# Kernel tuning notes

Measured on AMD Instinct MI355X. Metric: run time of the kernel, lower is better.

## Reference

```python
import jax, jax.numpy as jnp
import numpy as np

B, Lq, Lk, E = 4, 512, 512, 128
D = 2 * E  # input feature dim = 2*encode_size


def setup_inputs() -> dict:
    key = jax.random.key(0)
    ks = jax.random.split(key, 6)
    return {
        "query": jax.random.normal(ks[0], (B, Lq, D), jnp.float32),
        "key": jax.random.normal(ks[1], (B, Lk, D), jnp.float32),
        "value": jax.random.normal(ks[2], (B, Lq, D), jnp.float32),
        "Wc1": jax.random.normal(ks[3], (D, E), jnp.float32) / np.sqrt(D),
        "Wc2": jax.random.normal(ks[4], (D, E), jnp.float32) / np.sqrt(D),
        "vc": jax.random.normal(ks[5], (E,), jnp.float32) / np.sqrt(E),
    }


def reference(query, key, value, Wc1, Wc2, vc):
    # q: [B, Lq, E], k: [B, Lk, E]
    q = query @ Wc1
    k = key @ Wc2
    # additive (Bahdanau) scores: tanh(q + k) reduced by vc -> [B, Lk, Lq]
    sjt = jnp.einsum('blqe,e->blq', jnp.tanh(q[:, None, :, :] + k[:, :, None, :]), vc)
    atten = jax.nn.softmax(sjt, axis=2)  # softmax over Lq (dim=2), dropout p=0.0 is identity
    context = jnp.einsum('blq,bqd->bld', atten, value)  # [B, Lk, D]
    return (context, atten)
```

## Files before the change

### kernel.cpp

```cpp
#include <hip/hip_runtime.h>

#define NB 4
#define LQ 512
#define LK 512
#define EE 128
#define DD 256

__device__ __forceinline__ float fast_rcp(float x) { return __builtin_amdgcn_rcpf(x); }

__global__ __launch_bounds__(256) void proj_exp_kernel(
    const float* __restrict__ query, const float* __restrict__ key,
    const float* __restrict__ Wc1, const float* __restrict__ Wc2,
    float* __restrict__ EqT, float* __restrict__ Ek)
{
    __shared__ float in_s[8][DD];
    const int r0 = blockIdx.x * 8;
    const bool is_q = (r0 < NB * LQ);
    const float* src = is_q ? query : key;
    const float* W   = is_q ? Wc1   : Wc2;
    const int rbase  = is_q ? r0    : r0 - NB * LQ;

    const float4* srow4 = (const float4*)(src + (size_t)rbase * DD);
    #pragma unroll
    for (int i = 0; i < 2; ++i)
        ((float4*)in_s)[i * 256 + threadIdx.x] = srow4[i * 256 + threadIdx.x];
    __syncthreads();

    const int c  = threadIdx.x & 127;
    const int rg = threadIdx.x >> 7;
    float acc[4] = {0.f, 0.f, 0.f, 0.f};
    for (int d = 0; d < DD; d += 8) {
        const float w0 = W[(d + 0) * EE + c];
        const float w1 = W[(d + 1) * EE + c];
        const float w2 = W[(d + 2) * EE + c];
        const float w3 = W[(d + 3) * EE + c];
        const float w4 = W[(d + 4) * EE + c];
        const float w5 = W[(d + 5) * EE + c];
        const float w6 = W[(d + 6) * EE + c];
        const float w7 = W[(d + 7) * EE + c];
        #pragma unroll
        for (int i = 0; i < 4; ++i) {
            const float4 xa = *(const float4*)&in_s[rg * 4 + i][d];
            const float4 xb = *(const float4*)&in_s[rg * 4 + i][d + 4];
            acc[i] += xa.x * w0 + xa.y * w1 + xa.z * w2 + xa.w * w3
                    + xb.x * w4 + xb.y * w5 + xb.z * w6 + xb.w * w7;
        }
    }
    if (is_q) {
        const int b    = rbase >> 9;
        const int qloc = (rbase & 511) + rg * 4;
        float4 o;
        o.x = __expf(2.0f * acc[0]); o.y = __expf(2.0f * acc[1]);
        o.z = __expf(2.0f * acc[2]); o.w = __expf(2.0f * acc[3]);
        *(float4*)&EqT[((size_t)(b * EE + c)) * LQ + qloc] = o;
    } else {
        #pragma unroll
        for (int i = 0; i < 4; ++i)
            Ek[(size_t)(rbase + rg * 4 + i) * EE + c] = __expf(2.0f * acc[i]);
    }
}

__global__ __launch_bounds__(512) void atten_kernel(
    const float* __restrict__ EqT, const float* __restrict__ Ek,
    const float* __restrict__ vc, float* __restrict__ attn)
{
    __shared__ float  ek_s[4][EE];
    __shared__ float  vc_s[EE];
    __shared__ float  s2p_s[4][4][LQ];
    __shared__ float  sj_s[4][LQ];
    __shared__ float2 mZ_s[4][2];
    __shared__ float  scale_s[4][2];
    const int b   = blockIdx.x >> 7;
    const int lt  = blockIdx.x & 127;
    const int l0  = lt * 4;
    const int tid = threadIdx.x;
    const int qq  = tid & 127;
    const int eg  = tid >> 7;

    ((float*)ek_s)[tid] = Ek[((size_t)b * LK + l0) * EE + tid];
    if (tid < EE) vc_s[tid] = vc[tid];
    __syncthreads();

    float vcsum = 0.f;
    #pragma unroll
    for (int e = 0; e < EE; e += 4) {
        const float4 v = *(const float4*)&vc_s[e];
        vcsum += (v.x + v.y) + (v.z + v.w);
    }

    const float4* eq4 = (const float4*)(EqT + (size_t)b * EE * LQ);
    float s2[4][4];
    #pragma unroll
    for (int l = 0; l < 4; ++l) { s2[l][0]=0.f; s2[l][1]=0.f; s2[l][2]=0.f; s2[l][3]=0.f; }

    #pragma unroll 4
    for (int i = 0; i < 32; ++i) {
        const int e = eg * 32 + i;
        const float4 a  = eq4[(size_t)e * 128 + qq];
        const float  vv = vc_s[e];
        #pragma unroll
        for (int l = 0; l < 4; ++l) {
            const float kk = ek_s[l][e];
            s2[l][0] += vv * fast_rcp(a.x * kk + 1.0f);
            s2[l][1] += vv * fast_rcp(a.y * kk + 1.0f);
            s2[l][2] += vv * fast_rcp(a.z * kk + 1.0f);
            s2[l][3] += vv * fast_rcp(a.w * kk + 1.0f);
        }
    }

    #pragma unroll
    for (int l = 0; l < 4; ++l)
        *(float4*)&s2p_s[eg][l][qq * 4] =
            make_float4(s2[l][0], s2[l][1], s2[l][2], s2[l][3]);
    __syncthreads();

    const int w = tid >> 6, lane = tid & 63;
    const int l = w & 3, h2 = w >> 2, base = h2 * 256;
    float sjv[4];
    float m = -1e30f;
    #pragma unroll
    for (int i = 0; i < 4; ++i) {
        const int idx = base + lane + 64 * i;
        const float p = s2p_s[0][l][idx] + s2p_s[1][l][idx]
                      + s2p_s[2][l][idx] + s2p_s[3][l][idx];
        sjv[i] = vcsum - 2.0f * p;
        m = fmaxf(m, sjv[i]);
    }
    #pragma unroll
    for (int off = 32; off >= 1; off >>= 1) m = fmaxf(m, __shfl_xor(m, off));
    float Z = 0.f;
    #pragma unroll
    for (int i = 0; i < 4; ++i) {
        const int idx = base + lane + 64 * i;
        const float ex = __expf(sjv[i] - m);
        sj_s[l][idx] = ex;
        Z += ex;
    }
    #pragma unroll
    for (int off = 32; off >= 1; off >>= 1) Z += __shfl_xor(Z, off);
    if (lane == 0) mZ_s[l][h2] = make_float2(m, Z);
    __syncthreads();
    if (lane == 0) {
        const float2 A = mZ_s[l][0], B2 = mZ_s[l][1];
        const float M  = fmaxf(A.x, B2.x);
        const float Zt = A.y * __expf(A.x - M) + B2.y * __expf(B2.x - M);
        scale_s[l][h2] = __expf((h2 ? B2.x : A.x) - M) * fast_rcp(Zt);
    }
    __syncthreads();

    const int q = tid;
    #pragma unroll
    for (int li = 0; li < 4; ++li)
        attn[(size_t)(b * LK + l0 + li) * LQ + q] = sj_s[li][q] * scale_s[li][q >> 8];
}

__global__ __launch_bounds__(1024) void context_kernel(
    const float* __restrict__ attn, const float* __restrict__ value,
    float* __restrict__ ctx)
{
    const int b    = blockIdx.x >> 6;
    const int lt   = blockIdx.x & 63;
    const int row0 = b * LK + lt * 8;
    const int tid  = threadIdx.x;
    const int g    = tid >> 6;
    const int lane = tid & 63;
    const float4* v4 = (const float4*)(value + (size_t)b * LQ * DD);

    float4 ac[8];
    #pragma unroll
    for (int l = 0; l < 8; ++l) ac[l] = make_float4(0.f, 0.f, 0.f, 0.f);

    const int q0 = g * 32;
    for (int q = q0; q < q0 + 32; q += 4) {
        float4 a[8];
        #pragma unroll
        for (int l = 0; l < 8; ++l)
            a[l] = *(const float4*)(attn + (size_t)(row0 + l) * LQ + q);
        const float4 v0 = v4[(size_t)(q + 0) * 64 + lane];
        const float4 v1 = v4[(size_t)(q + 1) * 64 + lane];
        const float4 v2 = v4[(size_t)(q + 2) * 64 + lane];
        const float4 v3 = v4[(size_t)(q + 3) * 64 + lane];
        #pragma unroll
        for (int l = 0; l < 8; ++l) {
            ac[l].x += a[l].x * v0.x; ac[l].y += a[l].x * v0.y;
            ac[l].z += a[l].x * v0.z; ac[l].w += a[l].x * v0.w;
            ac[l].x += a[l].y * v1.x; ac[l].y += a[l].y * v1.y;
            ac[l].z += a[l].y * v1.z; ac[l].w += a[l].y * v1.w;
            ac[l].x += a[l].z * v2.x; ac[l].y += a[l].z * v2.y;
            ac[l].z += a[l].z * v2.z; ac[l].w += a[l].z * v2.w;
            ac[l].x += a[l].w * v3.x; ac[l].y += a[l].w * v3.y;
            ac[l].z += a[l].w * v3.z; ac[l].w += a[l].w * v3.w;
        }
    }

    __shared__ float4 red[8][8][64];
    if (g >= 8) {
        #pragma unroll
        for (int l = 0; l < 8; ++l) red[g - 8][l][lane] = ac[l];
    }
    __syncthreads();
    if (g < 8) {
        #pragma unroll
        for (int l = 0; l < 8; ++l) {
            const float4 r = red[g][l][lane];
            ac[l].x += r.x; ac[l].y += r.y; ac[l].z += r.z; ac[l].w += r.w;
        }
    }
    __syncthreads();
    if (g >= 4 && g < 8) {
        #pragma unroll
        for (int l = 0; l < 8; ++l) red[g - 4][l][lane] = ac[l];
    }
    __syncthreads();
    if (g < 4) {
        #pragma unroll
        for (int l = 0; l < 8; ++l) {
            const float4 r = red[g][l][lane];
            ac[l].x += r.x; ac[l].y += r.y; ac[l].z += r.z; ac[l].w += r.w;
        }
    }
    __syncthreads();
    if (g == 2 || g == 3) {
        #pragma unroll
        for (int l = 0; l < 8; ++l) red[g - 2][l][lane] = ac[l];
    }
    __syncthreads();
    if (g < 2) {
        #pragma unroll
        for (int l = 0; l < 8; ++l) {
            const float4 r = red[g][l][lane];
            ac[l].x += r.x; ac[l].y += r.y; ac[l].z += r.z; ac[l].w += r.w;
        }
    }
    __syncthreads();
    if (g == 1) {
        #pragma unroll
        for (int l = 0; l < 8; ++l) red[0][l][lane] = ac[l];
    }
    __syncthreads();
    if (g == 0) {
        #pragma unroll
        for (int l = 0; l < 8; ++l) {
            const float4 r = red[0][l][lane];
            ac[l].x += r.x; ac[l].y += r.y; ac[l].z += r.z; ac[l].w += r.w;
            ((float4*)ctx)[(size_t)(row0 + l) * 64 + lane] = ac[l];
        }
    }
}

extern "C" void kernel_launch(void* const* d_in, const int* in_sizes, int n_in,
                              void* d_out, int out_size, void* d_ws, size_t ws_size,
                              hipStream_t stream) {
    const float* query = (const float*)d_in[0];
    const float* key   = (const float*)d_in[1];
    const float* value = (const float*)d_in[2];
    const float* Wc1   = (const float*)d_in[3];
    const float* Wc2   = (const float*)d_in[4];
    const float* vc    = (const float*)d_in[5];

    float* ctx  = (float*)d_out;
    float* attn = (float*)d_out + (size_t)NB * LK * DD;

    float* EqT = ctx;
    float* Ek  = ctx + (size_t)NB * LQ * EE;

    proj_exp_kernel<<<dim3(512), dim3(256), 0, stream>>>(query, key, Wc1, Wc2, EqT, Ek);
    atten_kernel<<<dim3(NB * (LK / 4)), dim3(512), 0, stream>>>(EqT, Ek, vc, attn);
    context_kernel<<<dim3(NB * (LK / 8)), dim3(1024), 0, stream>>>(attn, value, ctx);
}
```

Measured before the change: 120.4 us.

## Fuse projection, attention and context into one persistent kernel with grid barriers

Merges the three kernels into a single 256-block launch. Projection and attention are separated by a software grid barrier whose atomic counters live in the last slots of the attn output buffer. Softmax rows now stay in shared memory and feed the context product directly instead of being re-read from global memory. A second barrier protects the final attn element that doubles as a counter, and a tiny init kernel zeroes both counters. This removes launch gaps and the attn round trip, at the cost of relying on all 256 blocks being co-resident, which the launch does not guarantee, and of running fewer, larger blocks per stage.

```diff
diff --git a/kernel.cpp b/kernel.cpp
--- a/kernel.cpp
+++ b/kernel.cpp
@@ -5,80 +5,109 @@
 #define LK 512
 #define EE 128
 #define DD 256
+#define GRID_BLOCKS 256
+
+#define P2_IDX ((size_t)NB * LK * LQ - 1)
+#define P1_IDX ((size_t)NB * LK * LQ - 66)
 
 __device__ __forceinline__ float fast_rcp(float x) { return __builtin_amdgcn_rcpf(x); }
 
-__global__ __launch_bounds__(256) void proj_exp_kernel(
+__device__ __forceinline__ void grid_sync_once(unsigned* cnt) {
+    __threadfence();
+    __syncthreads();
+    if (threadIdx.x == 0) {
+        unsigned prev = __hip_atomic_fetch_add(cnt, 1u, __ATOMIC_ACQ_REL,
+                                               __HIP_MEMORY_SCOPE_AGENT);
+        if (prev != (unsigned)(GRID_BLOCKS - 1)) {
+            while (__hip_atomic_load(cnt, __ATOMIC_ACQUIRE,
+                                     __HIP_MEMORY_SCOPE_AGENT) < (unsigned)GRID_BLOCKS) {}
+        }
+    }
+    __syncthreads();
+    __threadfence();
+}
+
+__global__ __launch_bounds__(64) void init_barriers(float* attn) {
+    if (threadIdx.x == 0) {
+        ((unsigned*)attn)[P1_IDX] = 0u;
+        ((unsigned*)attn)[P2_IDX] = 0u;
+    }
+}
+
+__global__ __launch_bounds__(512) void fused_atten_kernel(
     const float* __restrict__ query, const float* __restrict__ key,
-    const float* __restrict__ Wc1, const float* __restrict__ Wc2,
-    float* __restrict__ EqT, float* __restrict__ Ek)
+    const float* __restrict__ value,
+    const float* __restrict__ Wc1,  const float* __restrict__ Wc2,
+    const float* __restrict__ vc,
+    float* __restrict__ EqT, float* __restrict__ Ek,
+    float* __restrict__ attn, float* __restrict__ ctx)
 {
-    __shared__ float in_s[8][DD];
-    const int r0 = blockIdx.x * 8;
-    const bool is_q = (r0 < NB * LQ);
-    const float* src = is_q ? query : key;
-    const float* W   = is_q ? Wc1   : Wc2;
-    const int rbase  = is_q ? r0    : r0 - NB * LQ;
-
-    const float4* srow4 = (const float4*)(src + (size_t)rbase * DD);
-    #pragma unroll
-    for (int i = 0; i < 2; ++i)
-        ((float4*)in_s)[i * 256 + threadIdx.x] = srow4[i * 256 + threadIdx.x];
-    __syncthreads();
-
-    const int c  = threadIdx.x & 127;
-    const int rg = threadIdx.x >> 7;
-    float acc[4] = {0.f, 0.f, 0.f, 0.f};
-    for (int d = 0; d < DD; d += 8) {
-        const float w0 = W[(d + 0) * EE + c];
-        const float w1 = W[(d + 1) * EE + c];
-        const float w2 = W[(d + 2) * EE + c];
-        const float w3 = W[(d + 3) * EE + c];
-        const float w4 = W[(d + 4) * EE + c];
-        const float w5 = W[(d + 5) * EE + c];
-        const float w6 = W[(d + 6) * EE + c];
-        const float w7 = W[(d + 7) * EE + c];
-        #pragma unroll
-        for (int i = 0; i < 4; ++i) {
-            const float4 xa = *(const float4*)&in_s[rg * 4 + i][d];
-            const float4 xb = *(const float4*)&in_s[rg * 4 + i][d + 4];
-            acc[i] += xa.x * w0 + xa.y * w1 + xa.z * w2 + xa.w * w3
-                    + xb.x * w4 + xb.y * w5 + xb.z * w6 + xb.w * w7;
-        }
-    }
-    if (is_q) {
-        const int b    = rbase >> 9;
-        const int qloc = (rbase & 511) + rg * 4;
-        float4 o;
-        o.x = __expf(2.0f * acc[0]); o.y = __expf(2.0f * acc[1]);
-        o.z = __expf(2.0f * acc[2]); o.w = __expf(2.0f * acc[3]);
-        *(float4*)&EqT[((size_t)(b * EE + c)) * LQ + qloc] = o;
-    } else {
-        #pragma unroll
-        for (int i = 0; i < 4; ++i)
-            Ek[(size_t)(rbase + rg * 4 + i) * EE + c] = __expf(2.0f * acc[i]);
-    }
-}
-
-__global__ __launch_bounds__(512) void atten_kernel(
-    const float* __restrict__ EqT, const float* __restrict__ Ek,
-    const float* __restrict__ vc, float* __restrict__ attn)
-{
-    __shared__ float  ek_s[4][EE];
-    __shared__ float  vc_s[EE];
-    __shared__ float  s2p_s[4][4][LQ];
-    __shared__ float  sj_s[4][LQ];
-    __shared__ float2 mZ_s[4][2];
-    __shared__ float  scale_s[4][2];
-    const int b   = blockIdx.x >> 7;
-    const int lt  = blockIdx.x & 127;
-    const int l0  = lt * 4;
+    __shared__ float in_s[16][DD];
+    __shared__ float ek_s[8][EE];
+    __shared__ float vc_s[EE];
+    __shared__ __align__(16) float s2p_s[4][8][LQ];
+    __shared__ float sj_s[8][LQ];
+
     const int tid = threadIdx.x;
-    const int qq  = tid & 127;
-    const int eg  = tid >> 7;
-
-    ((float*)ek_s)[tid] = Ek[((size_t)b * LK + l0) * EE + tid];
-    if (tid < EE) vc_s[tid] = vc[tid];
+
+    {
+        const int bid  = blockIdx.x;
+        const bool is_q = (bid < 128);
+        const int r0   = (is_q ? bid : bid - 128) * 16;
+        const float* src = is_q ? query : key;
+        const float* W   = is_q ? Wc1   : Wc2;
+
+        const float4* srow4 = (const float4*)(src + (size_t)r0 * DD);
+        #pragma unroll
+        for (int i = 0; i < 2; ++i)
+            ((float4*)in_s)[i * 512 + tid] = srow4[i * 512 + tid];
+        __syncthreads();
+
+        const int c  = tid & 127;
+        const int rg = tid >> 7;
+        float acc[4] = {0.f, 0.f, 0.f, 0.f};
+        for (int d = 0; d < DD; d += 8) {
+            const float w0 = W[(d + 0) * EE + c];
+            const float w1 = W[(d + 1) * EE + c];
+            const float w2 = W[(d + 2) * EE + c];
+            const float w3 = W[(d + 3) * EE + c];
+            const float w4 = W[(d + 4) * EE + c];
+            const float w5 = W[(d + 5) * EE + c];
+            const float w6 = W[(d + 6) * EE + c];
+            const float w7 = W[(d + 7) * EE + c];
+            #pragma unroll
+            for (int i = 0; i < 4; ++i) {
+                const float4 xa = *(const float4*)&in_s[rg * 4 + i][d];
+                const float4 xb = *(const float4*)&in_s[rg * 4 + i][d + 4];
+                acc[i] += xa.x * w0 + xa.y * w1 + xa.z * w2 + xa.w * w3
+                        + xb.x * w4 + xb.y * w5 + xb.z * w6 + xb.w * w7;
+            }
+        }
+        if (is_q) {
+            const int grow = r0 + rg * 4;
+            const int b    = grow >> 9;
+            const int qloc = grow & 511;
+            float4 o;
+            o.x = __expf(2.0f * acc[0]); o.y = __expf(2.0f * acc[1]);
+            o.z = __expf(2.0f * acc[2]); o.w = __expf(2.0f * acc[3]);
+            *(float4*)&EqT[((size_t)(b * EE + c)) * LQ + qloc] = o;
+        } else {
+            #pragma unroll
+            for (int i = 0; i < 4; ++i)
+                Ek[(size_t)(r0 + rg * 4 + i) * EE + c] = __expf(2.0f * acc[i]);
+        }
+    }
+    grid_sync_once((unsigned*)attn + P1_IDX);
+
+    const int b  = blockIdx.x >> 6;
+    const int lt = blockIdx.x & 63;
+    const int l0 = lt * 8;
+    {
+        const float* ekb = Ek + ((size_t)b * LK + l0) * EE;
+        ((float*)ek_s)[tid]       = ekb[tid];
+        ((float*)ek_s)[tid + 512] = ekb[tid + 512];
+        if (tid < EE) vc_s[tid] = vc[tid];
+    }
     __syncthreads();
 
     float vcsum = 0.f;
@@ -88,162 +117,141 @@
         vcsum += (v.x + v.y) + (v.z + v.w);
     }
 
-    const float4* eq4 = (const float4*)(EqT + (size_t)b * EE * LQ);
-    float s2[4][4];
-    #pragma unroll
-    for (int l = 0; l < 4; ++l) { s2[l][0]=0.f; s2[l][1]=0.f; s2[l][2]=0.f; s2[l][3]=0.f; }
-
-    #pragma unroll 4
-    for (int i = 0; i < 32; ++i) {
-        const int e = eg * 32 + i;
-        const float4 a  = eq4[(size_t)e * 128 + qq];
-        const float  vv = vc_s[e];
-        #pragma unroll
-        for (int l = 0; l < 4; ++l) {
-            const float kk = ek_s[l][e];
-            s2[l][0] += vv * fast_rcp(a.x * kk + 1.0f);
-            s2[l][1] += vv * fast_rcp(a.y * kk + 1.0f);
-            s2[l][2] += vv * fast_rcp(a.z * kk + 1.0f);
-            s2[l][3] += vv * fast_rcp(a.w * kk + 1.0f);
-        }
-    }
-
-    #pragma unroll
-    for (int l = 0; l < 4; ++l)
-        *(float4*)&s2p_s[eg][l][qq * 4] =
-            make_float4(s2[l][0], s2[l][1], s2[l][2], s2[l][3]);
+    {
+        const int qq = tid & 127;
+        const int eg = tid >> 7;
+        float s2[8][4];
+        #pragma unroll
+        for (int l = 0; l < 8; ++l)
+            { s2[l][0]=0.f; s2[l][1]=0.f; s2[l][2]=0.f; s2[l][3]=0.f; }
+
+        const float4* eq4 = (const float4*)(EqT + (size_t)b * EE * LQ);
+        #pragma unroll 2
+        for (int i = 0; i < 32; ++i) {
+            const int e = eg * 32 + i;
+            const float4 a  = eq4[(size_t)e * 128 + qq];
+            const float  vv = vc_s[e];
+            #pragma unroll
+            for (int l = 0; l < 8; ++l) {
+                const float kk = ek_s[l][e];
+                s2[l][0] += vv * fast_rcp(a.x * kk + 1.0f);
+                s2[l][1] += vv * fast_rcp(a.y * kk + 1.0f);
+                s2[l][2] += vv * fast_rcp(a.z * kk + 1.0f);
+                s2[l][3] += vv * fast_rcp(a.w * kk + 1.0f);
+            }
+        }
+        #pragma unroll
+        for (int l = 0; l < 8; ++l)
+            *(float4*)&s2p_s[eg][l][qq * 4] =
+                make_float4(s2[l][0], s2[l][1], s2[l][2], s2[l][3]);
+    }
     __syncthreads();
 
     const int w = tid >> 6, lane = tid & 63;
-    const int l = w & 3, h2 = w >> 2, base = h2 * 256;
-    float sjv[4];
-    float m = -1e30f;
-    #pragma unroll
-    for (int i = 0; i < 4; ++i) {
-        const int idx = base + lane + 64 * i;
-        const float p = s2p_s[0][l][idx] + s2p_s[1][l][idx]
-                      + s2p_s[2][l][idx] + s2p_s[3][l][idx];
-        sjv[i] = vcsum - 2.0f * p;
-        m = fmaxf(m, sjv[i]);
-    }
-    #pragma unroll
-    for (int off = 32; off >= 1; off >>= 1) m = fmaxf(m, __shfl_xor(m, off));
-    float Z = 0.f;
-    #pragma unroll
-    for (int i = 0; i < 4; ++i) {
-        const int idx = base + lane + 64 * i;
-        const float ex = __expf(sjv[i] - m);
-        sj_s[l][idx] = ex;
-        Z += ex;
-    }
-    #pragma unroll
-    for (int off = 32; off >= 1; off >>= 1) Z += __shfl_xor(Z, off);
-    if (lane == 0) mZ_s[l][h2] = make_float2(m, Z);
-    __syncthreads();
-    if (lane == 0) {
-        const float2 A = mZ_s[l][0], B2 = mZ_s[l][1];
-        const float M  = fmaxf(A.x, B2.x);
-        const float Zt = A.y * __expf(A.x - M) + B2.y * __expf(B2.x - M);
-        scale_s[l][h2] = __expf((h2 ? B2.x : A.x) - M) * fast_rcp(Zt);
-    }
-    __syncthreads();
-
-    const int q = tid;
-    #pragma unroll
-    for (int li = 0; li < 4; ++li)
-        attn[(size_t)(b * LK + l0 + li) * LQ + q] = sj_s[li][q] * scale_s[li][q >> 8];
-}
-
-__global__ __launch_bounds__(1024) void context_kernel(
-    const float* __restrict__ attn, const float* __restrict__ value,
-    float* __restrict__ ctx)
-{
-    const int b    = blockIdx.x >> 6;
-    const int lt   = blockIdx.x & 63;
-    const int row0 = b * LK + lt * 8;
-    const int tid  = threadIdx.x;
-    const int g    = tid >> 6;
-    const int lane = tid & 63;
-    const float4* v4 = (const float4*)(value + (size_t)b * LQ * DD);
-
-    float4 ac[8];
-    #pragma unroll
-    for (int l = 0; l < 8; ++l) ac[l] = make_float4(0.f, 0.f, 0.f, 0.f);
-
-    const int q0 = g * 32;
-    for (int q = q0; q < q0 + 32; q += 4) {
-        float4 a[8];
-        #pragma unroll
-        for (int l = 0; l < 8; ++l)
-            a[l] = *(const float4*)(attn + (size_t)(row0 + l) * LQ + q);
-        const float4 v0 = v4[(size_t)(q + 0) * 64 + lane];
-        const float4 v1 = v4[(size_t)(q + 1) * 64 + lane];
-        const float4 v2 = v4[(size_t)(q + 2) * 64 + lane];
-        const float4 v3 = v4[(size_t)(q + 3) * 64 + lane];
-        #pragma unroll
-        for (int l = 0; l < 8; ++l) {
-            ac[l].x += a[l].x * v0.x; ac[l].y += a[l].x * v0.y;
-            ac[l].z += a[l].x * v0.z; ac[l].w += a[l].x * v0.w;
-            ac[l].x += a[l].y * v1.x; ac[l].y += a[l].y * v1.y;
-            ac[l].z += a[l].y * v1.z; ac[l].w += a[l].y * v1.w;
-            ac[l].x += a[l].z * v2.x; ac[l].y += a[l].z * v2.y;
-            ac[l].z += a[l].z * v2.z; ac[l].w += a[l].z * v2.w;
-            ac[l].x += a[l].w * v3.x; ac[l].y += a[l].w * v3.y;
-            ac[l].z += a[l].w * v3.z; ac[l].w += a[l].w * v3.w;
-        }
-    }
-
-    __shared__ float4 red[8][8][64];
-    if (g >= 8) {
-        #pragma unroll
-        for (int l = 0; l < 8; ++l) red[g - 8][l][lane] = ac[l];
-    }
-    __syncthreads();
-    if (g < 8) {
-        #pragma unroll
-        for (int l = 0; l < 8; ++l) {
-            const float4 r = red[g][l][lane];
-            ac[l].x += r.x; ac[l].y += r.y; ac[l].z += r.z; ac[l].w += r.w;
-        }
-    }
-    __syncthreads();
-    if (g >= 4 && g < 8) {
-        #pragma unroll
-        for (int l = 0; l < 8; ++l) red[g - 4][l][lane] = ac[l];
-    }
-    __syncthreads();
-    if (g < 4) {
-        #pragma unroll
-        for (int l = 0; l < 8; ++l) {
-            const float4 r = red[g][l][lane];
-            ac[l].x += r.x; ac[l].y += r.y; ac[l].z += r.z; ac[l].w += r.w;
-        }
-    }
-    __syncthreads();
-    if (g == 2 || g == 3) {
-        #pragma unroll
-        for (int l = 0; l < 8; ++l) red[g - 2][l][lane] = ac[l];
-    }
-    __syncthreads();
-    if (g < 2) {
-        #pragma unroll
-        for (int l = 0; l < 8; ++l) {
-            const float4 r = red[g][l][lane];
-            ac[l].x += r.x; ac[l].y += r.y; ac[l].z += r.z; ac[l].w += r.w;
-        }
-    }
-    __syncthreads();
-    if (g == 1) {
-        #pragma unroll
-        for (int l = 0; l < 8; ++l) red[0][l][lane] = ac[l];
-    }
-    __syncthreads();
-    if (g == 0) {
-        #pragma unroll
-        for (int l = 0; l < 8; ++l) {
-            const float4 r = red[0][l][lane];
-            ac[l].x += r.x; ac[l].y += r.y; ac[l].z += r.z; ac[l].w += r.w;
-            ((float4*)ctx)[(size_t)(row0 + l) * 64 + lane] = ac[l];
+    {
+        float sjv[8], ex[8];
+        float m = -1e30f;
+        #pragma unroll
+        for (int i = 0; i < 8; ++i) {
+            const int idx = lane + 64 * i;
+            const float p = s2p_s[0][w][idx] + s2p_s[1][w][idx]
+                          + s2p_s[2][w][idx] + s2p_s[3][w][idx];
+            sjv[i] = vcsum - 2.0f * p;
+            m = fmaxf(m, sjv[i]);
+        }
+        #pragma unroll
+        for (int off = 32; off >= 1; off >>= 1) m = fmaxf(m, __shfl_xor(m, off));
+        float Z = 0.f;
+        #pragma unroll
+        for (int i = 0; i < 8; ++i) { ex[i] = __expf(sjv[i] - m); Z += ex[i]; }
+        #pragma unroll
+        for (int off = 32; off >= 1; off >>= 1) Z += __shfl_xor(Z, off);
+        const float rs = fast_rcp(Z);
+
+        float* arow = attn + ((size_t)(b * LK + l0 + w)) * LQ;
+        const bool p2owner = (blockIdx.x == GRID_BLOCKS - 1) && (tid == 511);
+        float keep = 0.f;
+        #pragma unroll
+        for (int i = 0; i < 8; ++i) {
+            const int idx = lane + 64 * i;
+            const float v = ex[i] * rs;
+            sj_s[w][idx] = v;
+            if (p2owner && i == 7) keep = v;
+            else                   arow[idx] = v;
+        }
+        grid_sync_once((unsigned*)attn + P2_IDX);
+        if (p2owner) arow[511] = keep;
+    }
+
+    {
+        const int g = w;
+        const float4* v4 = (const float4*)(value + (size_t)b * LQ * DD);
+        float4 ac[8];
+        #pragma unroll
+        for (int l = 0; l < 8; ++l) ac[l] = make_float4(0.f, 0.f, 0.f, 0.f);
+
+        const int q0 = g * 64;
+        for (int q = q0; q < q0 + 64; q += 4) {
+            float4 a[8];
+            #pragma unroll
+            for (int l = 0; l < 8; ++l)
+                a[l] = *(const float4*)&sj_s[l][q];
+            const float4 v0 = v4[(size_t)(q + 0) * 64 + lane];
+            const float4 v1 = v4[(size_t)(q + 1) * 64 + lane];
+            const float4 v2 = v4[(size_t)(q + 2) * 64 + lane];
+            const float4 v3 = v4[(size_t)(q + 3) * 64 + lane];
+            #pragma unroll
+            for (int l = 0; l < 8; ++l) {
+                ac[l].x += a[l].x * v0.x; ac[l].y += a[l].x * v0.y;
+                ac[l].z += a[l].x * v0.z; ac[l].w += a[l].x * v0.w;
+                ac[l].x += a[l].y * v1.x; ac[l].y += a[l].y * v1.y;
+                ac[l].z += a[l].y * v1.z; ac[l].w += a[l].y * v1.w;
+                ac[l].x += a[l].z * v2.x; ac[l].y += a[l].z * v2.y;
+                ac[l].z += a[l].z * v2.z; ac[l].w += a[l].z * v2.w;
+                ac[l].x += a[l].w * v3.x; ac[l].y += a[l].w * v3.y;
+                ac[l].z += a[l].w * v3.z; ac[l].w += a[l].w * v3.w;
+            }
+        }
+
+        float4 (*red)[8][64] = (float4 (*)[8][64])s2p_s;
+        if (g >= 4) {
+            #pragma unroll
+            for (int l = 0; l < 8; ++l) red[g - 4][l][lane] = ac[l];
+        }
+        __syncthreads();
+        if (g < 4) {
+            #pragma unroll
+            for (int l = 0; l < 8; ++l) {
+                const float4 r = red[g][l][lane];
+                ac[l].x += r.x; ac[l].y += r.y; ac[l].z += r.z; ac[l].w += r.w;
+            }
+        }
+        __syncthreads();
+        if (g == 2 || g == 3) {
+            #pragma unroll
+            for (int l = 0; l < 8; ++l) red[g - 2][l][lane] = ac[l];
+        }
+        __syncthreads();
+        if (g < 2) {
+            #pragma unroll
+            for (int l = 0; l < 8; ++l) {
+                const float4 r = red[g][l][lane];
+                ac[l].x += r.x; ac[l].y += r.y; ac[l].z += r.z; ac[l].w += r.w;
+            }
+        }
+        __syncthreads();
+        if (g == 1) {
+            #pragma unroll
+            for (int l = 0; l < 8; ++l) red[0][l][lane] = ac[l];
+        }
+        __syncthreads();
+        if (g == 0) {
+            #pragma unroll
+            for (int l = 0; l < 8; ++l) {
+                const float4 r = red[0][l][lane];
+                ac[l].x += r.x; ac[l].y += r.y; ac[l].z += r.z; ac[l].w += r.w;
+                ((float4*)ctx)[(size_t)(b * LK + l0 + l) * 64 + lane] = ac[l];
+            }
         }
     }
 }
@@ -264,7 +272,7 @@
     float* EqT = ctx;
     float* Ek  = ctx + (size_t)NB * LQ * EE;
 
-    proj_exp_kernel<<<dim3(512), dim3(256), 0, stream>>>(query, key, Wc1, Wc2, EqT, Ek);
-    atten_kernel<<<dim3(NB * (LK / 4)), dim3(512), 0, stream>>>(EqT, Ek, vc, attn);
-    context_kernel<<<dim3(NB * (LK / 8)), dim3(1024), 0, stream>>>(attn, value, ctx);
-}
+    init_barriers<<<dim3(1), dim3(64), 0, stream>>>(attn);
+    fused_atten_kernel<<<dim3(GRID_BLOCKS), dim3(512), 0, stream>>>(
+        query, key, value, Wc1, Wc2, vc, EqT, Ek, attn, ctx);
+}
```

Result: slower. 295.2 us (+145.3%).
